# Optimization experiments

Hardware: AMD Instinct MI355X
Metric: run time of the kernel (lower is better)

The kernel has to match this reference:

```python
import jax, jax.numpy as jnp
import numpy as np

B, S, D = 2, 2048, 768
H = 12
DH = D // H
EPS = 1e-12


def setup_inputs() -> dict:
    key = jax.random.key(0)
    ks = jax.random.split(key, 16)
    s = 0.02
    return {
        "hidden_states": jax.random.normal(ks[0], (B, S, D), jnp.float32),
        "attention_mask": jnp.zeros((B, 1, 1, S), jnp.float32),
        "position_bias": jax.random.normal(ks[1], (1, H, S, S), jnp.float32),
        "q_w": jax.random.normal(ks[2], (D, D), jnp.float32) * s,
        "q_b": jnp.zeros((D,), jnp.float32),
        "k_w": jax.random.normal(ks[3], (D, D), jnp.float32) * s,
        "k_b": jnp.zeros((D,), jnp.float32),
        "v_w": jax.random.normal(ks[4], (D, D), jnp.float32) * s,
        "v_b": jnp.zeros((D,), jnp.float32),
        "o_w": jax.random.normal(ks[5], (D, D), jnp.float32) * s,
        "o_b": jnp.zeros((D,), jnp.float32),
        "ln_w": jnp.ones((D,), jnp.float32),
        "ln_b": jnp.zeros((D,), jnp.float32),
    }


def _split_heads(x):
    # [B, S, D] -> [B, H, S, DH]
    b, s, _ = x.shape
    return x.reshape(b, s, H, DH).transpose(0, 2, 1, 3)


def reference(hidden_states, attention_mask, position_bias,
              q_w, q_b, k_w, k_b, v_w, v_b, o_w, o_b, ln_w, ln_b):
    # nn.Linear: y = x @ W.T + b (W stored [out, in])
    q = _split_heads(hidden_states @ q_w.T + q_b)
    k = _split_heads(hidden_states @ k_w.T + k_b)
    v = _split_heads(hidden_states @ v_w.T + v_b)

    scale = 1.0 / jnp.sqrt(jnp.asarray(DH, hidden_states.dtype))
    scores = jnp.einsum('bhqd,bhkd->bhqk', q, k) * scale
    scores = scores + position_bias + attention_mask
    probs = jax.nn.softmax(scores, axis=-1)

    c = jnp.einsum('bhqk,bhkd->bhqd', probs, v)
    c = c.transpose(0, 2, 1, 3).reshape(hidden_states.shape[0], -1, D)
    o = c @ o_w.T + o_b

    # residual + LayerNorm (dropout is identity at eval)
    x = o + hidden_states
    mu = jnp.mean(x, axis=-1, keepdims=True)
    var = jnp.mean(jnp.square(x - mu), axis=-1, keepdims=True)
    out = (x - mu) * jax.lax.rsqrt(var + EPS) * ln_w + ln_b
    return out
```

## Files before the change

kernel.cpp:

```cpp
#include <hip/hip_runtime.h>
#include <math.h>

typedef unsigned short u16;
typedef float f32x4 __attribute__((ext_vector_type(4)));
typedef __bf16 bf16x8 __attribute__((ext_vector_type(8)));

#define B_ 2
#define S_ 2048
#define D_ 768
#define H_ 12
#define DH_ 64

__device__ __forceinline__ u16 f2bf(float x) {
  union { float f; unsigned u; } v; v.f = x;
  unsigned r = v.u + 0x7fffu + ((v.u >> 16) & 1u);
  return (u16)(r >> 16);
}

__device__ __forceinline__ f32x4 zero4() { f32x4 z = {0.f, 0.f, 0.f, 0.f}; return z; }

__device__ __forceinline__ f32x4 mfma16(bf16x8 a, bf16x8 b, f32x4 c) {
  return __builtin_amdgcn_mfma_f32_16x16x32_bf16(a, b, c, 0, 0, 0);
}

__device__ __forceinline__ void gload_lds16(const void* g, void* l) {
  __builtin_amdgcn_global_load_lds((const __attribute__((address_space(1))) void*)g,
                                   (__attribute__((address_space(3))) void*)l, 16, 0, 0);
}

__global__ void cvt_kernel(const float* __restrict__ hid, const float* __restrict__ qw,
                           const float* __restrict__ kw, const float* __restrict__ vw,
                           const float* __restrict__ ow, u16* __restrict__ Hb,
                           u16* __restrict__ Wb) {
  const int NH = B_ * S_ * D_;
  const int NW = D_ * D_;
  const int T4 = (NH + 4 * NW) >> 2;
  int stride = gridDim.x * blockDim.x;
  for (int i = blockIdx.x * blockDim.x + threadIdx.x; i < T4; i += stride) {
    int e = i << 2;
    const float* src; u16* dst;
    if (e < NH) { src = hid + e; dst = Hb + e; }
    else {
      int o = e - NH;
      int m = o / NW, oo = o - m * NW;
      src = (m == 0 ? qw : m == 1 ? kw : m == 2 ? vw : ow) + oo;
      dst = Wb + o;
    }
    f32x4 v = *(const f32x4*)src;
    uint2 o2;
    o2.x = (unsigned)f2bf(v[0]) | ((unsigned)f2bf(v[1]) << 16);
    o2.y = (unsigned)f2bf(v[2]) | ((unsigned)f2bf(v[3]) << 16);
    *(uint2*)dst = o2;
  }
}

#define BM 128
#define BN 128
#define BK 64

__global__ __launch_bounds__(256) void gemm_kernel(
    const u16* __restrict__ A, const u16* __restrict__ W,
    const float* __restrict__ bq, const float* __restrict__ bk, const float* __restrict__ bv,
    u16* __restrict__ Qb, u16* __restrict__ Kb, u16* __restrict__ Vtmp,
    float* __restrict__ Of, const float* __restrict__ bO, int mode)
{
  __shared__ __align__(16) u16 As[BM * BK];
  __shared__ __align__(16) u16 Bs[BN * BK];
  int t = threadIdx.x;
  int lane = t & 63, w = t >> 6;
  int wr = w >> 1, wc = w & 1;
  int l15 = lane & 15, l4 = lane >> 4;
  int m0 = blockIdx.y * BM, n0 = blockIdx.x * BN;

  f32x4 acc[4][4];
#pragma unroll
  for (int i = 0; i < 4; ++i)
#pragma unroll
    for (int j = 0; j < 4; ++j) acc[i][j] = zero4();

  const int K = D_;
  for (int k0 = 0; k0 < K; k0 += BK) {
    __syncthreads();
#pragma unroll
    for (int p = 0; p < 4; ++p) {
      int seg = p * 4 + w;
      int bd = seg * 64 + lane;
      int row = bd >> 3;
      int slot = (bd & 7) ^ (row & 7);
      gload_lds16(A + (size_t)(m0 + row) * K + k0 + slot * 8, (char*)As + seg * 1024);
      gload_lds16(W + (size_t)(n0 + row) * K + k0 + slot * 8, (char*)Bs + seg * 1024);
    }
    __syncthreads();
#pragma unroll
    for (int kk = 0; kk < 2; ++kk) {
      bf16x8 af[4], bfr[4];
#pragma unroll
      for (int i = 0; i < 4; ++i) {
        int ra = wr * 64 + i * 16 + l15;
        af[i] = *(const bf16x8*)((const char*)As + ra * 128 +
                                 ((kk * 64 + (l4 << 4)) ^ ((ra & 7) << 4)));
        int rb = wc * 64 + i * 16 + l15;
        bfr[i] = *(const bf16x8*)((const char*)Bs + rb * 128 +
                                  ((kk * 64 + (l4 << 4)) ^ ((rb & 7) << 4)));
      }
#pragma unroll
      for (int i = 0; i < 4; ++i)
#pragma unroll
        for (int j = 0; j < 4; ++j)
          acc[i][j] = mfma16(af[i], bfr[j], acc[i][j]);
    }
  }

  if (mode == 0) {
    int mat = n0 / D_;
    int ncol0 = (n0 - mat * D_) + wc * 64;
    const float* bias = (mat == 0) ? bq : (mat == 1 ? bk : bv);
    u16* outp = (mat == 0) ? Qb : (mat == 1 ? Kb : Vtmp);
    float scale = (mat == 0) ? 0.125f : 1.0f;
    int h = ncol0 >> 6;
#pragma unroll
    for (int j = 0; j < 4; ++j) {
      int d = j * 16 + l15;
      float bvv = bias[ncol0 + d];
#pragma unroll
      for (int i = 0; i < 4; ++i) {
#pragma unroll
        for (int r = 0; r < 4; ++r) {
          int m = m0 + wr * 64 + i * 16 + (l4 << 2) + r;
          int bb = m >> 11, ss = m & 2047;
          float val = (acc[i][j][r] + bvv) * scale;
          outp[(((size_t)bb * H_ + h) * S_ + ss) * DH_ + d] = f2bf(val);
        }
      }
    }
  } else {
#pragma unroll
    for (int j = 0; j < 4; ++j) {
      int n = n0 + wc * 64 + j * 16 + l15;
      float bvv = bO[n];
#pragma unroll
      for (int i = 0; i < 4; ++i) {
#pragma unroll
        for (int r = 0; r < 4; ++r) {
          int m = m0 + wr * 64 + i * 16 + (l4 << 2) + r;
          Of[(size_t)m * D_ + n] = acc[i][j][r] + bvv;
        }
      }
    }
  }
}

__global__ __launch_bounds__(256) void vtrans_kernel(const u16* __restrict__ V,
                                                     u16* __restrict__ Vt) {
  __shared__ __align__(16) u16 tile[64 * 64];
  int t = threadIdx.x;
  int s0 = blockIdx.x * 64;
  int bh = blockIdx.y;
  const u16* src = V + ((size_t)bh * S_ + s0) * DH_;
#pragma unroll
  for (int p = 0; p < 2; ++p) {
    int bd = t + p * 256;
    int row = bd >> 3, slot = bd & 7;
    uint4 v = *(const uint4*)(src + row * 64 + slot * 8);
    *(uint4*)((char*)tile + row * 128 + ((slot ^ (row & 7)) << 4)) = v;
  }
  __syncthreads();
  int d = t >> 2, sc = (t & 3) * 16;
  u16* dst = Vt + ((size_t)bh * DH_ + d) * S_ + s0 + sc;
  int colB = d * 2;
#pragma unroll
  for (int half = 0; half < 2; ++half) {
    u16 tmp[8] __attribute__((aligned(16)));
#pragma unroll
    for (int j = 0; j < 8; ++j) {
      int s = sc + half * 8 + j;
      tmp[j] = *(const u16*)((const char*)tile + s * 128 +
                             (((colB >> 4) ^ (s & 7)) << 4) + (colB & 15));
    }
    *(uint4*)(dst + half * 8) = *(const uint4*)tmp;
  }
}

__global__ __launch_bounds__(512, 6) void attn_kernel(
    const u16* __restrict__ Qb, const u16* __restrict__ Kb, const u16* __restrict__ Vt,
    const float* __restrict__ bias, const float* __restrict__ mask, u16* __restrict__ Cb)
{
  __shared__ __align__(16) u16 Ks[2][64 * 64];
  __shared__ __align__(16) u16 Vs[2][64 * 64];
  __shared__ __align__(16) char upool[17408];
  u16 (*Ps)[16][72] = (u16 (*)[16][72])upool;
  float (*Osh)[16][66] = (float (*)[16][66])upool;
  float (*Lsh)[2][16] = (float (*)[2][16])(upool + 16896);

  int t = threadIdx.x, lane = t & 63, w = t >> 6;
  int qg = w & 3, kg = w >> 2;
  int q0 = blockIdx.x * 64, h = blockIdx.y, b = blockIdx.z;
  size_t bh = (size_t)b * H_ + h;
  const u16* Qp = Qb + (bh * S_ + q0) * DH_;
  const u16* Kp = Kb + bh * S_ * DH_;
  const u16* Vp = Vt + bh * DH_ * S_;
  const float* biasp = bias + ((size_t)h * S_ + q0) * S_;
  const float* maskp = mask + (size_t)b * S_;
  int l15 = lane & 15, l4 = lane >> 4;
  int kc0 = kg * 32;

  const float* brp0 = biasp + (size_t)(qg * 16 + (l4 << 2) + 0) * S_ + kc0 + l15;
  const float* brp1 = brp0 + S_;
  const float* brp2 = brp1 + S_;
  const float* brp3 = brp2 + S_;
  const float* mkp = maskp + kc0 + l15;

  bf16x8 qf0, qf1;
  {
    const u16* qrow = Qp + (qg * 16 + l15) * DH_;
    qf0 = *(const bf16x8*)(qrow + l4 * 8);
    qf1 = *(const bf16x8*)(qrow + 32 + l4 * 8);
  }

  f32x4 oacc[4];
#pragma unroll
  for (int i = 0; i < 4; ++i) oacc[i] = zero4();
  float lrow[4] = {0.f, 0.f, 0.f, 0.f};

  float bc0[2], bc1[2], bc2[2], bc3[2];
  float bn0[2], bn1[2], bn2[2], bn3[2];

  {
    int row = t >> 3;
    int slot = (t & 7) ^ (row & 7);
    gload_lds16(Kp + (size_t)row * DH_ + slot * 8, (char*)Ks[0] + w * 1024);
    gload_lds16(Vp + (size_t)row * S_ + slot * 8, (char*)Vs[0] + w * 1024);
  }
#pragma unroll
  for (int kf = 0; kf < 2; ++kf) {
    float mk = mkp[kf * 16];
    bc0[kf] = brp0[kf * 16] + mk;
    bc1[kf] = brp1[kf * 16] + mk;
    bc2[kf] = brp2[kf * 16] + mk;
    bc3[kf] = brp3[kf * 16] + mk;
  }
  __syncthreads();

  int cur = 0;
  for (int kt = 0; kt < S_ / 64; ++kt) {
    int k0 = kt * 64;
    if (kt + 1 < S_ / 64) {
      int k0n = k0 + 64;
      int row = t >> 3;
      int slot = (t & 7) ^ (row & 7);
      gload_lds16(Kp + (size_t)(k0n + row) * DH_ + slot * 8, (char*)Ks[cur ^ 1] + w * 1024);
      gload_lds16(Vp + (size_t)row * S_ + k0n + slot * 8, (char*)Vs[cur ^ 1] + w * 1024);
#pragma unroll
      for (int kf = 0; kf < 2; ++kf) {
        float mk = mkp[k0n + kf * 16];
        bn0[kf] = brp0[k0n + kf * 16] + mk;
        bn1[kf] = brp1[k0n + kf * 16] + mk;
        bn2[kf] = brp2[k0n + kf * 16] + mk;
        bn3[kf] = brp3[k0n + kf * 16] + mk;
      }
    }

    const u16* Kc = Ks[cur];
    const u16* Vc = Vs[cur];

    f32x4 sf[2];
#pragma unroll
    for (int kf = 0; kf < 2; ++kf) {
      int row = kc0 + kf * 16 + l15;
      bf16x8 kb0 = *(const bf16x8*)((const char*)Kc + row * 128 +
                                    ((l4 << 4) ^ ((row & 7) << 4)));
      bf16x8 kb1 = *(const bf16x8*)((const char*)Kc + row * 128 +
                                    ((64 + (l4 << 4)) ^ ((row & 7) << 4)));
      f32x4 s0 = zero4();
      s0 = mfma16(qf0, kb0, s0);
      s0 = mfma16(qf1, kb1, s0);
      sf[kf] = s0;
    }

#pragma unroll
    for (int kf = 0; kf < 2; ++kf) {
      float p0 = __expf(sf[kf][0] + bc0[kf]);
      float p1 = __expf(sf[kf][1] + bc1[kf]);
      float p2 = __expf(sf[kf][2] + bc2[kf]);
      float p3 = __expf(sf[kf][3] + bc3[kf]);
      sf[kf][0] = p0; sf[kf][1] = p1; sf[kf][2] = p2; sf[kf][3] = p3;
      lrow[0] += p0; lrow[1] += p1; lrow[2] += p2; lrow[3] += p3;
    }

#pragma unroll
    for (int r = 0; r < 4; ++r)
#pragma unroll
      for (int kf = 0; kf < 2; ++kf)
        Ps[qg][(l4 << 2) + r][kc0 + kf * 16 + l15] = f2bf(sf[kf][r]);

    bf16x8 pa = *(const bf16x8*)&Ps[qg][l15][kc0 + l4 * 8];

#pragma unroll
    for (int df = 0; df < 4; ++df) {
      int row = df * 16 + l15;
      bf16x8 vb = *(const bf16x8*)((const char*)Vc + row * 128 +
                                   ((kg * 64 + (l4 << 4)) ^ ((row & 7) << 4)));
      oacc[df] = mfma16(pa, vb, oacc[df]);
    }

    __syncthreads();
    cur ^= 1;
#pragma unroll
    for (int kf = 0; kf < 2; ++kf) {
      bc0[kf] = bn0[kf]; bc1[kf] = bn1[kf];
      bc2[kf] = bn2[kf]; bc3[kf] = bn3[kf];
    }
  }

#pragma unroll
  for (int r = 0; r < 4; ++r) {
#pragma unroll
    for (int o = 1; o < 16; o <<= 1) lrow[r] += __shfl_xor(lrow[r], o, 64);
  }
  if (l15 == 0) {
#pragma unroll
    for (int r = 0; r < 4; ++r) Lsh[qg][kg][(l4 << 2) + r] = lrow[r];
  }
  if (kg == 1) {
#pragma unroll
    for (int r = 0; r < 4; ++r)
#pragma unroll
      for (int df = 0; df < 4; ++df)
        Osh[qg][(l4 << 2) + r][df * 16 + l15] = oacc[df][r];
  }
  __syncthreads();
  if (kg == 0) {
#pragma unroll
    for (int r = 0; r < 4; ++r) {
      int rr = (l4 << 2) + r;
      float inv = 1.0f / (Lsh[qg][0][rr] + Lsh[qg][1][rr]);
      int q = q0 + qg * 16 + rr;
      size_t base = ((size_t)b * S_ + q) * D_ + h * DH_ + l15;
#pragma unroll
      for (int df = 0; df < 4; ++df)
        Cb[base + df * 16] = f2bf((oacc[df][r] + Osh[qg][rr][df * 16 + l15]) * inv);
    }
  }
}

__global__ __launch_bounds__(192) void ln_kernel(const float* __restrict__ O,
                                                 const float* __restrict__ hid,
                                                 const float* __restrict__ lw,
                                                 const float* __restrict__ lb,
                                                 float* __restrict__ out) {
  int row = blockIdx.x, t = threadIdx.x;
  size_t base = (size_t)row * D_;
  f32x4 x = *(const f32x4*)(O + base + t * 4);
  f32x4 hh = *(const f32x4*)(hid + base + t * 4);
  x = x + hh;
  float s = x[0] + x[1] + x[2] + x[3];
  float s2 = x[0] * x[0] + x[1] * x[1] + x[2] * x[2] + x[3] * x[3];
#pragma unroll
  for (int o = 1; o < 64; o <<= 1) {
    s += __shfl_xor(s, o, 64);
    s2 += __shfl_xor(s2, o, 64);
  }
  __shared__ float rs[3], rs2[3];
  int w = t >> 6, lane = t & 63;
  if (lane == 0) { rs[w] = s; rs2[w] = s2; }
  __syncthreads();
  s = rs[0] + rs[1] + rs[2];
  s2 = rs2[0] + rs2[1] + rs2[2];
  float mu = s * (1.0f / 768.0f);
  float var = s2 * (1.0f / 768.0f) - mu * mu;
  float rstd = rsqrtf(var + 1e-12f);
  f32x4 w4 = *(const f32x4*)(lw + t * 4);
  f32x4 b4 = *(const f32x4*)(lb + t * 4);
  f32x4 y = (x - mu) * rstd * w4 + b4;
  *(f32x4*)(out + base + t * 4) = y;
}

extern "C" void kernel_launch(void* const* d_in, const int* in_sizes, int n_in,
                              void* d_out, int out_size, void* d_ws, size_t ws_size,
                              hipStream_t stream) {
  const float* hid  = (const float*)d_in[0];
  const float* mask = (const float*)d_in[1];
  const float* bias = (const float*)d_in[2];
  const float* qw = (const float*)d_in[3];
  const float* qb = (const float*)d_in[4];
  const float* kw = (const float*)d_in[5];
  const float* kb = (const float*)d_in[6];
  const float* vw = (const float*)d_in[7];
  const float* vb = (const float*)d_in[8];
  const float* ow = (const float*)d_in[9];
  const float* ob = (const float*)d_in[10];
  const float* lnw = (const float*)d_in[11];
  const float* lnb = (const float*)d_in[12];

  char* ws = (char*)d_ws;
  const size_t NHB = (size_t)B_ * S_ * D_ * 2;
  const size_t NWB = (size_t)4 * D_ * D_ * 2;
  const size_t NQB = (size_t)B_ * H_ * S_ * DH_ * 2;
  u16* Hb = (u16*)ws;
  u16* Wb = (u16*)(ws + NHB);
  u16* Qb = (u16*)(ws + NHB + NWB);
  u16* Kb = (u16*)(ws + NHB + NWB + NQB);
  u16* Vt = (u16*)(ws + NHB + NWB + 2 * NQB);
  u16* Cb = (u16*)(ws + NHB + NWB + 3 * NQB);
  float* Of = (float*)(ws + NHB + NWB + 4 * NQB);
  u16* Vtmp = (u16*)Of;

  cvt_kernel<<<2048, 256, 0, stream>>>(hid, qw, kw, vw, ow, Hb, Wb);

  gemm_kernel<<<dim3(18, 32), 256, 0, stream>>>(
      Hb, Wb, qb, kb, vb, Qb, Kb, Vtmp, nullptr, nullptr, 0);

  vtrans_kernel<<<dim3(S_ / 64, B_ * H_), 256, 0, stream>>>(Vtmp, Vt);

  attn_kernel<<<dim3(S_ / 64, H_, B_), 512, 0, stream>>>(Qb, Kb, Vt, bias, mask, Cb);

  gemm_kernel<<<dim3(6, 32), 256, 0, stream>>>(
      Cb, Wb + (size_t)3 * D_ * D_, nullptr, nullptr, nullptr,
      nullptr, nullptr, nullptr, Of, ob, 1);

  ln_kernel<<<B_ * S_, 192, 0, stream>>>(Of, hid, lnw, lnb, (float*)d_out);
}
```

Before: 149.8 us.

## Unroll attention loop by two with vmcnt-gated barriers and XCD-aware block mapping

The attention kernel's K-tile loop is unrolled by two, with ping-pong bias register sets instead of copying them each iteration. The full __syncthreads is replaced by a partial s_waitcnt vmcnt plus a raw s_barrier, so some loads can stay in flight across the barrier. The grid is flattened to 1D and blocks are remapped so that both batches of the same head/query tile land on the same XCD, sharing the position_bias and K/V reads in its L2. The main risk is correctness of the hand-counted vmcnt value, since a wrong count could let a tile be read before its load lands.

```diff
diff --git a/kernel.cpp b/kernel.cpp
--- a/kernel.cpp
+++ b/kernel.cpp
@@ -192,15 +192,20 @@
   float (*Osh)[16][66] = (float (*)[16][66])upool;
   float (*Lsh)[2][16] = (float (*)[2][16])(upool + 16896);
 
-  int t = threadIdx.x, lane = t & 63, w = t >> 6;
+  int t = threadIdx.x, w = t >> 6;
   int qg = w & 3, kg = w >> 2;
-  int q0 = blockIdx.x * 64, h = blockIdx.y, b = blockIdx.z;
+  int id = blockIdx.x;
+  int xcd = id & 7, rest = id >> 3;
+  int b = rest & 1, p_ = xcd + 8 * (rest >> 1);
+  int xq = p_ & 31, h = p_ >> 5;
+  int q0 = xq * 64;
   size_t bh = (size_t)b * H_ + h;
   const u16* Qp = Qb + (bh * S_ + q0) * DH_;
   const u16* Kp = Kb + bh * S_ * DH_;
   const u16* Vp = Vt + bh * DH_ * S_;
   const float* biasp = bias + ((size_t)h * S_ + q0) * S_;
   const float* maskp = mask + (size_t)b * S_;
+  int lane = t & 63;
   int l15 = lane & 15, l4 = lane >> 4;
   int kc0 = kg * 32;
 
@@ -222,47 +227,29 @@
   for (int i = 0; i < 4; ++i) oacc[i] = zero4();
   float lrow[4] = {0.f, 0.f, 0.f, 0.f};
 
-  float bc0[2], bc1[2], bc2[2], bc3[2];
-  float bn0[2], bn1[2], bn2[2], bn3[2];
-
-  {
+  float bA0[2], bA1[2], bA2[2], bA3[2];
+  float bB0[2], bB1[2], bB2[2], bB3[2];
+
+  auto STAGE = [&](int kt, int sb) {
     int row = t >> 3;
     int slot = (t & 7) ^ (row & 7);
-    gload_lds16(Kp + (size_t)row * DH_ + slot * 8, (char*)Ks[0] + w * 1024);
-    gload_lds16(Vp + (size_t)row * S_ + slot * 8, (char*)Vs[0] + w * 1024);
-  }
-#pragma unroll
-  for (int kf = 0; kf < 2; ++kf) {
-    float mk = mkp[kf * 16];
-    bc0[kf] = brp0[kf * 16] + mk;
-    bc1[kf] = brp1[kf * 16] + mk;
-    bc2[kf] = brp2[kf * 16] + mk;
-    bc3[kf] = brp3[kf * 16] + mk;
-  }
-  __syncthreads();
-
-  int cur = 0;
-  for (int kt = 0; kt < S_ / 64; ++kt) {
-    int k0 = kt * 64;
-    if (kt + 1 < S_ / 64) {
-      int k0n = k0 + 64;
-      int row = t >> 3;
-      int slot = (t & 7) ^ (row & 7);
-      gload_lds16(Kp + (size_t)(k0n + row) * DH_ + slot * 8, (char*)Ks[cur ^ 1] + w * 1024);
-      gload_lds16(Vp + (size_t)row * S_ + k0n + slot * 8, (char*)Vs[cur ^ 1] + w * 1024);
-#pragma unroll
-      for (int kf = 0; kf < 2; ++kf) {
-        float mk = mkp[k0n + kf * 16];
-        bn0[kf] = brp0[k0n + kf * 16] + mk;
-        bn1[kf] = brp1[k0n + kf * 16] + mk;
-        bn2[kf] = brp2[k0n + kf * 16] + mk;
-        bn3[kf] = brp3[k0n + kf * 16] + mk;
-      }
-    }
-
-    const u16* Kc = Ks[cur];
-    const u16* Vc = Vs[cur];
-
+    gload_lds16(Kp + (size_t)(kt * 64 + row) * DH_ + slot * 8, (char*)Ks[sb] + w * 1024);
+    gload_lds16(Vp + (size_t)row * S_ + kt * 64 + slot * 8, (char*)Vs[sb] + w * 1024);
+  };
+  auto PREFETCH = [&](float (&c0)[2], float (&c1)[2], float (&c2)[2], float (&c3)[2],
+                      int kt) {
+    int kb = kt * 64;
+#pragma unroll
+    for (int kf = 0; kf < 2; ++kf) {
+      float mk = mkp[kb + kf * 16];
+      c0[kf] = brp0[kb + kf * 16] + mk;
+      c1[kf] = brp1[kb + kf * 16] + mk;
+      c2[kf] = brp2[kb + kf * 16] + mk;
+      c3[kf] = brp3[kb + kf * 16] + mk;
+    }
+  };
+  auto COMPUTE = [&](const u16* Kc, const u16* Vc,
+                     float (&c0)[2], float (&c1)[2], float (&c2)[2], float (&c3)[2]) {
     f32x4 sf[2];
 #pragma unroll
     for (int kf = 0; kf < 2; ++kf) {
@@ -276,25 +263,21 @@
       s0 = mfma16(qf1, kb1, s0);
       sf[kf] = s0;
     }
-
 #pragma unroll
     for (int kf = 0; kf < 2; ++kf) {
-      float p0 = __expf(sf[kf][0] + bc0[kf]);
-      float p1 = __expf(sf[kf][1] + bc1[kf]);
-      float p2 = __expf(sf[kf][2] + bc2[kf]);
-      float p3 = __expf(sf[kf][3] + bc3[kf]);
+      float p0 = __expf(sf[kf][0] + c0[kf]);
+      float p1 = __expf(sf[kf][1] + c1[kf]);
+      float p2 = __expf(sf[kf][2] + c2[kf]);
+      float p3 = __expf(sf[kf][3] + c3[kf]);
       sf[kf][0] = p0; sf[kf][1] = p1; sf[kf][2] = p2; sf[kf][3] = p3;
       lrow[0] += p0; lrow[1] += p1; lrow[2] += p2; lrow[3] += p3;
     }
-
 #pragma unroll
     for (int r = 0; r < 4; ++r)
 #pragma unroll
       for (int kf = 0; kf < 2; ++kf)
         Ps[qg][(l4 << 2) + r][kc0 + kf * 16 + l15] = f2bf(sf[kf][r]);
-
     bf16x8 pa = *(const bf16x8*)&Ps[qg][l15][kc0 + l4 * 8];
-
 #pragma unroll
     for (int df = 0; df < 4; ++df) {
       int row = df * 16 + l15;
@@ -302,15 +285,39 @@
                                    ((kg * 64 + (l4 << 4)) ^ ((row & 7) << 4)));
       oacc[df] = mfma16(pa, vb, oacc[df]);
     }
-
-    __syncthreads();
+  };
+
+#define PIPE_BARRIER() do {                                  \
+    asm volatile("s_waitcnt vmcnt(10)" ::: "memory");        \
+    __builtin_amdgcn_s_barrier();                            \
+    __builtin_amdgcn_sched_barrier(0);                       \
+  } while (0)
+
+  STAGE(0, 0);
+  __builtin_amdgcn_sched_barrier(0);
+  PREFETCH(bA0, bA1, bA2, bA3, 0);
+  PIPE_BARRIER();
+
+  int cur = 0;
+  for (int kt = 0; kt < S_ / 64; kt += 2) {
+    STAGE(kt + 1, cur ^ 1);
+    __builtin_amdgcn_sched_barrier(0);
+    PREFETCH(bB0, bB1, bB2, bB3, kt + 1);
+    COMPUTE(Ks[cur], Vs[cur], bA0, bA1, bA2, bA3);
+    PIPE_BARRIER();
     cur ^= 1;
-#pragma unroll
-    for (int kf = 0; kf < 2; ++kf) {
-      bc0[kf] = bn0[kf]; bc1[kf] = bn1[kf];
-      bc2[kf] = bn2[kf]; bc3[kf] = bn3[kf];
-    }
-  }
+    if (kt + 2 < S_ / 64) {
+      STAGE(kt + 2, cur ^ 1);
+      __builtin_amdgcn_sched_barrier(0);
+      PREFETCH(bA0, bA1, bA2, bA3, kt + 2);
+    } else {
+      __builtin_amdgcn_sched_barrier(0);
+    }
+    COMPUTE(Ks[cur], Vs[cur], bB0, bB1, bB2, bB3);
+    PIPE_BARRIER();
+    cur ^= 1;
+  }
+#undef PIPE_BARRIER
 
 #pragma unroll
   for (int r = 0; r < 4; ++r) {
@@ -412,7 +419,7 @@
 
   vtrans_kernel<<<dim3(S_ / 64, B_ * H_), 256, 0, stream>>>(Vtmp, Vt);
 
-  attn_kernel<<<dim3(S_ / 64, H_, B_), 512, 0, stream>>>(Qb, Kb, Vt, bias, mask, Cb);
+  attn_kernel<<<dim3(768), 512, 0, stream>>>(Qb, Kb, Vt, bias, mask, Cb);
 
   gemm_kernel<<<dim3(6, 32), 256, 0, stream>>>(
       Cb, Wb + (size_t)3 * D_ * D_, nullptr, nullptr, nullptr,
```

Measured after the change: 199.6 us. 1.33x slower.

## Stage position bias tiles into LDS via async global-to-LDS double buffering

Applied to the files above, without the earlier changes.

Position bias is now fetched per 64x64 tile with direct global-to-LDS 16-byte loads into a swizzled, double-buffered shared buffer. This replaces the per-thread scalar register prefetch, which used strided 4-byte loads per row. The goal is coalesced, wide loads of the dominant bias stream, overlapped with compute like K/V. In exchange LDS use grows by about 32KB, occupancy hint drops from 6 to 4, and Ps gets its own buffer, adding extra LDS reads per tile.

```diff
diff --git a/kernel.cpp b/kernel.cpp
--- a/kernel.cpp
+++ b/kernel.cpp
@@ -181,16 +181,16 @@
   }
 }
 
-__global__ __launch_bounds__(512, 6) void attn_kernel(
+__global__ __launch_bounds__(512, 4) void attn_kernel(
     const u16* __restrict__ Qb, const u16* __restrict__ Kb, const u16* __restrict__ Vt,
     const float* __restrict__ bias, const float* __restrict__ mask, u16* __restrict__ Cb)
 {
   __shared__ __align__(16) u16 Ks[2][64 * 64];
   __shared__ __align__(16) u16 Vs[2][64 * 64];
-  __shared__ __align__(16) char upool[17408];
-  u16 (*Ps)[16][72] = (u16 (*)[16][72])upool;
-  float (*Osh)[16][66] = (float (*)[16][66])upool;
-  float (*Lsh)[2][16] = (float (*)[2][16])(upool + 16896);
+  __shared__ __align__(16) char Bls[2][16384];
+  __shared__ __align__(16) u16 Ps[4][16][72];
+  float (*Osh)[16][66] = (float (*)[16][66])&Bls[0][0];
+  float (*Lsh)[2][16] = (float (*)[2][16])(&Bls[0][0] + 16896);
 
   int t = threadIdx.x, lane = t & 63, w = t >> 6;
   int qg = w & 3, kg = w >> 2;
@@ -204,12 +204,6 @@
   int l15 = lane & 15, l4 = lane >> 4;
   int kc0 = kg * 32;
 
-  const float* brp0 = biasp + (size_t)(qg * 16 + (l4 << 2) + 0) * S_ + kc0 + l15;
-  const float* brp1 = brp0 + S_;
-  const float* brp2 = brp1 + S_;
-  const float* brp3 = brp2 + S_;
-  const float* mkp = maskp + kc0 + l15;
-
   bf16x8 qf0, qf1;
   {
     const u16* qrow = Qp + (qg * 16 + l15) * DH_;
@@ -222,46 +216,55 @@
   for (int i = 0; i < 4; ++i) oacc[i] = zero4();
   float lrow[4] = {0.f, 0.f, 0.f, 0.f};
 
-  float bc0[2], bc1[2], bc2[2], bc3[2];
-  float bn0[2], bn1[2], bn2[2], bn3[2];
-
-  {
+  auto STAGE_KV = [&](int kt, int sb) {
     int row = t >> 3;
     int slot = (t & 7) ^ (row & 7);
-    gload_lds16(Kp + (size_t)row * DH_ + slot * 8, (char*)Ks[0] + w * 1024);
-    gload_lds16(Vp + (size_t)row * S_ + slot * 8, (char*)Vs[0] + w * 1024);
-  }
-#pragma unroll
-  for (int kf = 0; kf < 2; ++kf) {
-    float mk = mkp[kf * 16];
-    bc0[kf] = brp0[kf * 16] + mk;
-    bc1[kf] = brp1[kf * 16] + mk;
-    bc2[kf] = brp2[kf * 16] + mk;
-    bc3[kf] = brp3[kf * 16] + mk;
-  }
+    gload_lds16(Kp + (size_t)(kt * 64 + row) * DH_ + slot * 8, (char*)Ks[sb] + w * 1024);
+    gload_lds16(Vp + (size_t)row * S_ + kt * 64 + slot * 8, (char*)Vs[sb] + w * 1024);
+  };
+  auto STAGE_BIAS = [&](int kt, int bb) {
+    int k0 = kt * 64;
+#pragma unroll
+    for (int p = 0; p < 2; ++p) {
+      int seg = p * 8 + w;
+      int row = seg * 4 + (lane >> 4);
+      int byt = ((lane & 15) << 4) ^ ((row & 7) << 4);
+      gload_lds16((const char*)(biasp + (size_t)row * S_ + k0) + byt,
+                  &Bls[bb][0] + seg * 1024);
+    }
+  };
+
+  float mcur[2], mnxt[2];
+
+  STAGE_KV(0, 0);
+  STAGE_BIAS(0, 0);
+#pragma unroll
+  for (int kf = 0; kf < 2; ++kf) mcur[kf] = maskp[kc0 + kf * 16 + l15];
   __syncthreads();
 
-  int cur = 0;
   for (int kt = 0; kt < S_ / 64; ++kt) {
-    int k0 = kt * 64;
     if (kt + 1 < S_ / 64) {
-      int k0n = k0 + 64;
-      int row = t >> 3;
-      int slot = (t & 7) ^ (row & 7);
-      gload_lds16(Kp + (size_t)(k0n + row) * DH_ + slot * 8, (char*)Ks[cur ^ 1] + w * 1024);
-      gload_lds16(Vp + (size_t)row * S_ + k0n + slot * 8, (char*)Vs[cur ^ 1] + w * 1024);
-#pragma unroll
-      for (int kf = 0; kf < 2; ++kf) {
-        float mk = mkp[k0n + kf * 16];
-        bn0[kf] = brp0[k0n + kf * 16] + mk;
-        bn1[kf] = brp1[k0n + kf * 16] + mk;
-        bn2[kf] = brp2[k0n + kf * 16] + mk;
-        bn3[kf] = brp3[k0n + kf * 16] + mk;
+      STAGE_KV(kt + 1, (kt + 1) & 1);
+      STAGE_BIAS(kt + 1, (kt + 1) & 1);
+#pragma unroll
+      for (int kf = 0; kf < 2; ++kf)
+        mnxt[kf] = maskp[(kt + 1) * 64 + kc0 + kf * 16 + l15];
+    }
+
+    const u16* Kc = Ks[kt & 1];
+    const u16* Vc = Vs[kt & 1];
+    const char* Bc = &Bls[kt & 1][0];
+
+    float bcv[2][4];
+#pragma unroll
+    for (int kf = 0; kf < 2; ++kf) {
+      int col = kc0 + kf * 16 + l15;
+#pragma unroll
+      for (int r = 0; r < 4; ++r) {
+        int row = qg * 16 + (l4 << 2) + r;
+        bcv[kf][r] = *(const float*)(Bc + row * 256 + ((col << 2) ^ ((row & 7) << 4)));
       }
     }
-
-    const u16* Kc = Ks[cur];
-    const u16* Vc = Vs[cur];
 
     f32x4 sf[2];
 #pragma unroll
@@ -279,10 +282,10 @@
 
 #pragma unroll
     for (int kf = 0; kf < 2; ++kf) {
-      float p0 = __expf(sf[kf][0] + bc0[kf]);
-      float p1 = __expf(sf[kf][1] + bc1[kf]);
-      float p2 = __expf(sf[kf][2] + bc2[kf]);
-      float p3 = __expf(sf[kf][3] + bc3[kf]);
+      float p0 = __expf(sf[kf][0] + bcv[kf][0] + mcur[kf]);
+      float p1 = __expf(sf[kf][1] + bcv[kf][1] + mcur[kf]);
+      float p2 = __expf(sf[kf][2] + bcv[kf][2] + mcur[kf]);
+      float p3 = __expf(sf[kf][3] + bcv[kf][3] + mcur[kf]);
       sf[kf][0] = p0; sf[kf][1] = p1; sf[kf][2] = p2; sf[kf][3] = p3;
       lrow[0] += p0; lrow[1] += p1; lrow[2] += p2; lrow[3] += p3;
     }
@@ -304,12 +307,7 @@
     }
 
     __syncthreads();
-    cur ^= 1;
-#pragma unroll
-    for (int kf = 0; kf < 2; ++kf) {
-      bc0[kf] = bn0[kf]; bc1[kf] = bn1[kf];
-      bc2[kf] = bn2[kf]; bc3[kf] = bn3[kf];
-    }
+    mcur[0] = mnxt[0]; mcur[1] = mnxt[1];
   }
 
 #pragma unroll
```

Measured after the change: 173.0 us. 1.15x slower.

## Stage K/V through registers and prefetch bias two tiles ahead in attention loop

Applied to the files above, without the earlier changes.

Replaces the direct global-to-LDS async loads for K/V tiles with register-staged loads issued two iterations ahead, then stored to the alternate LDS buffer. Position-bias and mask loads are also prefetched two tiles ahead using A/B register sets alternated by iteration parity, and the mask is added at use time instead of at load time. The aim is to hide global latency of the bias stream and K/V loads behind more compute. In exchange it raises register pressure and adds an extra VGPR-to-LDS store path, and the parity branch duplicates the softmax code.

```diff
diff --git a/kernel.cpp b/kernel.cpp
--- a/kernel.cpp
+++ b/kernel.cpp
@@ -210,6 +210,11 @@
   const float* brp3 = brp2 + S_;
   const float* mkp = maskp + kc0 + l15;
 
+  int srow = t >> 3, sslot = t & 7;
+  const u16* gK = Kp + (size_t)srow * DH_ + sslot * 8;
+  const u16* gV = Vp + (size_t)srow * S_ + sslot * 8;
+  int lofs = srow * 128 + ((sslot ^ (srow & 7)) << 4);
+
   bf16x8 qf0, qf1;
   {
     const u16* qrow = Qp + (qg * 16 + l15) * DH_;
@@ -222,41 +227,34 @@
   for (int i = 0; i < 4; ++i) oacc[i] = zero4();
   float lrow[4] = {0.f, 0.f, 0.f, 0.f};
 
-  float bc0[2], bc1[2], bc2[2], bc3[2];
-  float bn0[2], bn1[2], bn2[2], bn3[2];
-
-  {
-    int row = t >> 3;
-    int slot = (t & 7) ^ (row & 7);
-    gload_lds16(Kp + (size_t)row * DH_ + slot * 8, (char*)Ks[0] + w * 1024);
-    gload_lds16(Vp + (size_t)row * S_ + slot * 8, (char*)Vs[0] + w * 1024);
-  }
-#pragma unroll
-  for (int kf = 0; kf < 2; ++kf) {
-    float mk = mkp[kf * 16];
-    bc0[kf] = brp0[kf * 16] + mk;
-    bc1[kf] = brp1[kf * 16] + mk;
-    bc2[kf] = brp2[kf * 16] + mk;
-    bc3[kf] = brp3[kf * 16] + mk;
-  }
+  float bsA[4][2], mA[2];
+  float bsB[4][2], mB[2];
+#define LOADSET(BS, MM, kt) do { int kb = (kt) * 64;                         \
+    _Pragma("unroll") for (int kf = 0; kf < 2; ++kf) {                       \
+      BS[0][kf] = brp0[kb + kf * 16]; BS[1][kf] = brp1[kb + kf * 16];        \
+      BS[2][kf] = brp2[kb + kf * 16]; BS[3][kf] = brp3[kb + kf * 16];        \
+      MM[kf] = mkp[kb + kf * 16]; } } while (0)
+
+  uint4 stK, stV;
+
+  stK = *(const uint4*)gK;
+  stV = *(const uint4*)gV;
+  LOADSET(bsA, mA, 0);
+  LOADSET(bsB, mB, 1);
+  *(uint4*)((char*)Ks[0] + lofs) = stK;
+  *(uint4*)((char*)Vs[0] + lofs) = stV;
+  stK = *(const uint4*)(gK + 4096);
+  stV = *(const uint4*)(gV + 64);
   __syncthreads();
 
-  int cur = 0;
   for (int kt = 0; kt < S_ / 64; ++kt) {
-    int k0 = kt * 64;
+    int cur = kt & 1;
     if (kt + 1 < S_ / 64) {
-      int k0n = k0 + 64;
-      int row = t >> 3;
-      int slot = (t & 7) ^ (row & 7);
-      gload_lds16(Kp + (size_t)(k0n + row) * DH_ + slot * 8, (char*)Ks[cur ^ 1] + w * 1024);
-      gload_lds16(Vp + (size_t)row * S_ + k0n + slot * 8, (char*)Vs[cur ^ 1] + w * 1024);
-#pragma unroll
-      for (int kf = 0; kf < 2; ++kf) {
-        float mk = mkp[k0n + kf * 16];
-        bn0[kf] = brp0[k0n + kf * 16] + mk;
-        bn1[kf] = brp1[k0n + kf * 16] + mk;
-        bn2[kf] = brp2[k0n + kf * 16] + mk;
-        bn3[kf] = brp3[k0n + kf * 16] + mk;
+      *(uint4*)((char*)Ks[cur ^ 1] + lofs) = stK;
+      *(uint4*)((char*)Vs[cur ^ 1] + lofs) = stV;
+      if (kt + 2 < S_ / 64) {
+        stK = *(const uint4*)(gK + (size_t)(kt + 2) * 4096);
+        stV = *(const uint4*)(gV + (size_t)(kt + 2) * 64);
       }
     }
 
@@ -277,14 +275,28 @@
       sf[kf] = s0;
     }
 
-#pragma unroll
-    for (int kf = 0; kf < 2; ++kf) {
-      float p0 = __expf(sf[kf][0] + bc0[kf]);
-      float p1 = __expf(sf[kf][1] + bc1[kf]);
-      float p2 = __expf(sf[kf][2] + bc2[kf]);
-      float p3 = __expf(sf[kf][3] + bc3[kf]);
-      sf[kf][0] = p0; sf[kf][1] = p1; sf[kf][2] = p2; sf[kf][3] = p3;
-      lrow[0] += p0; lrow[1] += p1; lrow[2] += p2; lrow[3] += p3;
+    if ((kt & 1) == 0) {
+#pragma unroll
+      for (int kf = 0; kf < 2; ++kf) {
+        float p0 = __expf(sf[kf][0] + bsA[0][kf] + mA[kf]);
+        float p1 = __expf(sf[kf][1] + bsA[1][kf] + mA[kf]);
+        float p2 = __expf(sf[kf][2] + bsA[2][kf] + mA[kf]);
+        float p3 = __expf(sf[kf][3] + bsA[3][kf] + mA[kf]);
+        sf[kf][0] = p0; sf[kf][1] = p1; sf[kf][2] = p2; sf[kf][3] = p3;
+        lrow[0] += p0; lrow[1] += p1; lrow[2] += p2; lrow[3] += p3;
+      }
+      if (kt + 2 < S_ / 64) LOADSET(bsA, mA, kt + 2);
+    } else {
+#pragma unroll
+      for (int kf = 0; kf < 2; ++kf) {
+        float p0 = __expf(sf[kf][0] + bsB[0][kf] + mB[kf]);
+        float p1 = __expf(sf[kf][1] + bsB[1][kf] + mB[kf]);
+        float p2 = __expf(sf[kf][2] + bsB[2][kf] + mB[kf]);
+        float p3 = __expf(sf[kf][3] + bsB[3][kf] + mB[kf]);
+        sf[kf][0] = p0; sf[kf][1] = p1; sf[kf][2] = p2; sf[kf][3] = p3;
+        lrow[0] += p0; lrow[1] += p1; lrow[2] += p2; lrow[3] += p3;
+      }
+      if (kt + 2 < S_ / 64) LOADSET(bsB, mB, kt + 2);
     }
 
 #pragma unroll
@@ -304,13 +316,8 @@
     }
 
     __syncthreads();
-    cur ^= 1;
-#pragma unroll
-    for (int kf = 0; kf < 2; ++kf) {
-      bc0[kf] = bn0[kf]; bc1[kf] = bn1[kf];
-      bc2[kf] = bn2[kf]; bc3[kf] = bn3[kf];
-    }
-  }
+  }
+#undef LOADSET
 
 #pragma unroll
   for (int r = 0; r < 4; ++r) {
```

Result: slower. 342.8 us (+128.9%).
